# Kernel optimization log

Measured on AMD Instinct MI355X. Metric: run time of the kernel, lower is better.

Reference implementation:

```python
import jax, jax.numpy as jnp
import numpy as np

EPS = 1e-8          # torch nn.CosineSimilarity default eps
DIST_THR = 31.5     # 0.7 * 45 (module default)


def setup_inputs() -> dict:
    key = jax.random.key(0)
    k1, k2, k3, k4, k5 = jax.random.split(key, 5)
    B, C, H, W = 8, 256, 48, 48
    y = jax.random.normal(k1, (B, C, H, W), dtype=jnp.float32)
    yp = jax.random.normal(k2, (B, C, H, W), dtype=jnp.float32)
    z = jax.random.normal(k3, (B, C, H, W), dtype=jnp.float32)
    zp = jax.random.normal(k4, (B, C, H, W), dtype=jnp.float32)
    # distances in [0, 63): threshold 31.5 selects ~half of the pairs
    distances = jax.random.uniform(k5, (H, W, H, W), dtype=jnp.float32) * 63.0
    return {"y": y, "yp": yp, "z": z, "zp": zp, "distances": distances}


def _pairwise_cosine(a, b):
    # a, b: [B, C, N]; returns [B, N, N] cosine similarity over channel dim,
    # equivalent to CosineSimilarity(dim=1)(a[..., None], b[..., None, :])
    # but without materializing the [B, C, N, N] broadcast intermediate.
    dots = jnp.einsum('bcn,bcm->bnm', a, b)                       # [B,N,N]
    na = jnp.maximum(jnp.linalg.norm(a, axis=1), EPS)             # [B,N]
    nb = jnp.maximum(jnp.linalg.norm(b, axis=1), EPS)             # [B,N]
    return dots / (na[:, :, None] * nb[:, None, :])


def reference(y, yp, z, zp, distances):
    B, C = y.shape[0], y.shape[1]
    yf = y.reshape(B, C, -1)    # [B,C,N]
    ypf = yp.reshape(B, C, -1)
    zf = z.reshape(B, C, -1)
    zpf = zp.reshape(B, C, -1)

    cos_y_zp = _pairwise_cosine(yf, zpf)   # [B,N,N]
    cos_yp_z = _pairwise_cosine(zf, ypf)   # [B,N,N]

    H1, W1, H2, W2 = distances.shape
    mask = (distances.reshape(H1 * W1, H2 * W2) < DIST_THR)       # [N,N]

    # masked_select with mask broadcast over batch, then mean:
    # mean over B * count(mask) selected elements of -(cos1 + cos2)
    s = jnp.sum(jnp.where(mask[None, :, :], cos_y_zp + cos_yp_z, 0.0))
    cnt = jnp.sum(mask).astype(s.dtype) * B
    return -s / cnt
```

## Files before the change

kernel.cpp:

```cpp
#include <hip/hip_runtime.h>
#include <stdint.h>

#define GLOBAL_AS __attribute__((address_space(1)))
#define LDS_AS __attribute__((address_space(3)))

typedef _Float16 half_t;
typedef _Float16 f16x8 __attribute__((ext_vector_type(8)));
typedef float f32x4 __attribute__((ext_vector_type(4)));

static constexpr int BATCH = 8;
static constexpr int CH = 256;
static constexpr int N = 2304;
static constexpr int KTOT = 4096;
static constexpr int MW = 72;
static constexpr int MWORDS = 165888;
static constexpr int LROW = 258;
static constexpr float EPS = 1e-8f;
static constexpr float THR = 31.5f;


__global__ __launch_bounds__(256) void prep_kernel(
    const float* __restrict__ y, const float* __restrict__ yp,
    const float* __restrict__ z, const float* __restrict__ zp,
    const float* __restrict__ dist,
    half_t* __restrict__ At, half_t* __restrict__ Bt,
    uint32_t* __restrict__ maskw, unsigned int* __restrict__ c_part) {
  const int t = threadIdx.x;
  const int bz = blockIdx.z;

  if (bz >= 4) {
    const int blk = ((bz - 4) * 8 + blockIdx.y) * 36 + blockIdx.x;
    const int w = blk * 256 + t;
    int c = 0;
    if (w < MWORDS) {
      const float4* p = (const float4*)(dist + (size_t)w * 32);
      uint32_t bits = 0;
#pragma unroll
      for (int q = 0; q < 8; ++q) {
        float4 v = p[q];
        bits |= (v.x < THR ? 1u : 0u) << (q * 4);
        bits |= (v.y < THR ? 1u : 0u) << (q * 4 + 1);
        bits |= (v.z < THR ? 1u : 0u) << (q * 4 + 2);
        bits |= (v.w < THR ? 1u : 0u) << (q * 4 + 3);
      }
      maskw[w] = bits;
      c = __popc(bits);
    }
#pragma unroll
    for (int off = 32; off; off >>= 1) c += __shfl_down(c, off, 64);
    __shared__ int mred[4];
    if ((t & 63) == 0) mred[t >> 6] = c;
    __syncthreads();
    if (t == 0)
      c_part[blk] = (unsigned int)(mred[0] + mred[1] + mred[2] + mred[3]);
    return;
  }

  const int b = blockIdx.y;
  const int n0 = blockIdx.x * 64;
  const float* src; half_t* dst; int kh;
  switch (bz) {
    case 0:  src = y;  dst = At; kh = 0;    break;
    case 1:  src = z;  dst = At; kh = 2048; break;
    case 2:  src = zp; dst = Bt; kh = 0;    break;
    default: src = yp; dst = Bt; kh = 2048; break;
  }
  const int kbase = kh + b * 256;
  const int col4 = (t & 15) * 4;
  const int cb = t >> 4;

  const float* base = src + (size_t)(b * CH + cb * 16) * N + n0 + col4;
  float4 v[16];
#pragma unroll
  for (int i = 0; i < 16; ++i) v[i] = *(const float4*)(base + (size_t)i * N);

  float ss[4] = {0.f, 0.f, 0.f, 0.f};
#pragma unroll
  for (int i = 0; i < 16; ++i) {
    ss[0] = fmaf(v[i].x, v[i].x, ss[0]);
    ss[1] = fmaf(v[i].y, v[i].y, ss[1]);
    ss[2] = fmaf(v[i].z, v[i].z, ss[2]);
    ss[3] = fmaf(v[i].w, v[i].w, ss[3]);
  }
  __shared__ float partial[16][65];
  __shared__ float sc[64];
  __shared__ half_t tile[64 * LROW];
#pragma unroll
  for (int j = 0; j < 4; ++j) partial[cb][col4 + j] = ss[j];
  __syncthreads();
  if (t < 64) {
    float s = 0.f;
#pragma unroll
    for (int k = 0; k < 16; ++k) s += partial[k][t];
    sc[t] = 1.0f / fmaxf(sqrtf(s), EPS);
  }
  __syncthreads();

#pragma unroll
  for (int j = 0; j < 4; ++j) {
    const float scj = sc[col4 + j];
    union { half_t h[16]; f16x8 v2[2]; } u;
#pragma unroll
    for (int i = 0; i < 16; ++i)
      u.h[i] = (half_t)(((const float*)&v[i])[j] * scj);
    f16x8* q = (f16x8*)(tile + (col4 + j) * LROW + cb * 16);
    q[0] = u.v2[0];
    q[1] = u.v2[1];
  }
  __syncthreads();

  {
    const int r = t >> 4, c = t & 15;
#pragma unroll
    for (int p = 0; p < 4; ++p) {
      const int row = p * 16 + r;
      half_t* gout = dst + (size_t)(n0 + row) * KTOT + kbase;
      const half_t* lrow = tile + row * LROW;
#pragma unroll
      for (int inst = 0; inst < 2; ++inst) {
        const int off = c * 8 + inst * 128;
        *(f16x8*)(gout + off) = *(const f16x8*)(lrow + off);
      }
    }
  }
}

__global__ __launch_bounds__(256, 2) void gemm_kernel(
    const half_t* __restrict__ At, const half_t* __restrict__ Bt,
    const uint32_t* __restrict__ maskw, float* __restrict__ s_part) {
  __shared__ half_t As[128 * 64];
  __shared__ half_t Bs[256 * 64];
  __shared__ float red[4];

  const int t = threadIdx.x;
  const int lane = t & 63;
  const int w = t >> 6;

  const int bi = blockIdx.x;
  const int zt = bi & 7;
  const int v  = bi >> 3;
  const int nt = v / 9;
  const int mt = v % 9;
  const int m0 = mt * 256;
  const int n0 = nt * 128;
  const int k0 = zt * 512;

  const int srow = lane >> 3;
  const int schunk = ((lane & 7) ^ ((lane >> 3) & 7)) * 8;
  const half_t* gA = At + (size_t)(n0 + w * 32 + srow) * KTOT + k0 + schunk;
  const half_t* gB = Bt + (size_t)(m0 + w * 64 + srow) * KTOT + k0 + schunk;
  half_t* lA = As + (w * 32) * 64;
  half_t* lB = Bs + (w * 64) * 64;

  const int wm = (w & 1) * 64;
  const int wn = (w >> 1) * 128;
  const int fra = wm + (lane & 15);
  const int frb = wn + (lane & 15);
  const int fk0 = (((lane >> 4)    ) ^ (lane & 7)) * 8;
  const int fk1 = ((4 + (lane >> 4)) ^ (lane & 7)) * 8;

  f32x4 acc[4][8] = {};

  for (int kt = 0; kt < 8; ++kt) {
    const half_t* ga = gA + kt * 64;
    const half_t* gb = gB + kt * 64;
#pragma unroll
    for (int i = 0; i < 4; ++i)
      __builtin_amdgcn_global_load_lds((const GLOBAL_AS void*)(ga + (size_t)(i * 8) * KTOT),
                                       (LDS_AS void*)(lA + i * 8 * 64), 16, 0, 0);
#pragma unroll
    for (int i = 0; i < 8; ++i)
      __builtin_amdgcn_global_load_lds((const GLOBAL_AS void*)(gb + (size_t)(i * 8) * KTOT),
                                       (LDS_AS void*)(lB + i * 8 * 64), 16, 0, 0);
    __syncthreads();
#pragma unroll
    for (int s = 0; s < 2; ++s) {
      const int fk = s ? fk1 : fk0;
      f16x8 af[4], bf[8];
#pragma unroll
      for (int i = 0; i < 4; ++i) af[i] = *(const f16x8*)(As + (fra + i * 16) * 64 + fk);
#pragma unroll
      for (int j = 0; j < 8; ++j) bf[j] = *(const f16x8*)(Bs + (frb + j * 16) * 64 + fk);
#pragma unroll
      for (int i = 0; i < 4; ++i)
#pragma unroll
        for (int j = 0; j < 8; ++j)
          acc[i][j] = __builtin_amdgcn_mfma_f32_16x16x32_f16(af[i], bf[j], acc[i][j], 0, 0, 0);
    }
    __syncthreads();
  }

  float local = 0.f;
  const int mbase = (m0 + wn) >> 5;
  const int mbit = lane & 15;
#pragma unroll
  for (int i = 0; i < 4; ++i) {
    const int ng = n0 + wm + i * 16 + (lane >> 4) * 4;
#pragma unroll
    for (int r = 0; r < 4; ++r) {
      const uint4 wv = *(const uint4*)(maskw + (size_t)(ng + r) * MW + mbase);
      const uint32_t ww[4] = {wv.x, wv.y, wv.z, wv.w};
#pragma unroll
      for (int jp = 0; jp < 4; ++jp) {
        if ((ww[jp] >> mbit) & 1u)        local += acc[i][2 * jp][r];
        if ((ww[jp] >> (mbit + 16)) & 1u) local += acc[i][2 * jp + 1][r];
      }
    }
  }
#pragma unroll
  for (int off = 32; off; off >>= 1) local += __shfl_down(local, off, 64);
  if (lane == 0) red[w] = local;
  __syncthreads();
  if (t == 0) s_part[bi] = red[0] + red[1] + red[2] + red[3];
}

__global__ void finalize_kernel(const float* __restrict__ s_part,
                                const unsigned int* __restrict__ c_part,
                                float* __restrict__ out) {
  const int t = threadIdx.x;
  float local = 0.f;
  for (int i = t; i < 1296; i += 256) local += s_part[i];
  unsigned int clocal = 0;
  for (int i = t; i < 864; i += 256) clocal += c_part[i];
#pragma unroll
  for (int off = 32; off; off >>= 1) {
    local += __shfl_down(local, off, 64);
    clocal += __shfl_down(clocal, off, 64);
  }
  __shared__ float red[4];
  __shared__ unsigned int credu[4];
  if ((t & 63) == 0) { red[t >> 6] = local; credu[t >> 6] = clocal; }
  __syncthreads();
  if (t == 0) {
    const float s = red[0] + red[1] + red[2] + red[3];
    const float cnt = (float)(credu[0] + credu[1] + credu[2] + credu[3]);
    out[0] = -s / (cnt * (float)BATCH);
  }
}

extern "C" void kernel_launch(void* const* d_in, const int* in_sizes, int n_in,
                              void* d_out, int out_size, void* d_ws, size_t ws_size,
                              hipStream_t stream) {
  const float* y    = (const float*)d_in[0];
  const float* yp   = (const float*)d_in[1];
  const float* z    = (const float*)d_in[2];
  const float* zp   = (const float*)d_in[3];
  const float* dist = (const float*)d_in[4];
  float* out = (float*)d_out;

  char* ws = (char*)d_ws;
  float* s_part = (float*)ws;
  unsigned int* c_part = (unsigned int*)(ws + 8192);
  half_t* At = (half_t*)(ws + 16384);
  half_t* Bt = (half_t*)(ws + 16384 + 18874368);
  uint32_t* maskw = (uint32_t*)(ws + 16384 + 2 * 18874368);

  prep_kernel<<<dim3(36, 8, 7), 256, 0, stream>>>(y, yp, z, zp, dist, At, Bt, maskw, c_part);
  gemm_kernel<<<dim3(1296), 256, 0, stream>>>(At, Bt, maskw, s_part);
  finalize_kernel<<<1, 256, 0, stream>>>(s_part, c_part, out);
}
```

Baseline: 177.4 us.

## Restructure masked GEMM as 256x256 tiles with 4-stage LDS pipeline and 3-way split-K

The GEMM kernel moves from 1296 blocks of 128x256 tiles with 8-way split-K and a synchronous load-compute loop to 243 blocks of 512 threads computing 256x256 tiles with 3-way split-K. K steps of 32 go through a 4-buffer LDS ring filled by async global_load_lds, with explicit vmcnt waits, MFMA priority raising, and XCD-aware block remapping. The aim is to hide global load latency, raise data reuse per tile, and cut partial-sum overhead. In exchange it uses more LDS and registers per block, and 243 blocks may not fill all CUs evenly.

```diff
diff --git a/kernel.cpp b/kernel.cpp
--- a/kernel.cpp
+++ b/kernel.cpp
@@ -17,6 +17,7 @@
 static constexpr int LROW = 258;
 static constexpr float EPS = 1e-8f;
 static constexpr float THR = 31.5f;
+static constexpr int NBLK = 243;
 
 
 __global__ __launch_bounds__(256) void prep_kernel(
@@ -125,93 +126,111 @@
   }
 }
 
-__global__ __launch_bounds__(256, 2) void gemm_kernel(
+__global__ __launch_bounds__(512, 2) void gemm_kernel(
     const half_t* __restrict__ At, const half_t* __restrict__ Bt,
     const uint32_t* __restrict__ maskw, float* __restrict__ s_part) {
-  __shared__ half_t As[128 * 64];
-  __shared__ half_t Bs[256 * 64];
-  __shared__ float red[4];
+  __shared__ __align__(16) half_t As[4 * 8192];
+  __shared__ __align__(16) half_t Bs[4 * 8192];
+  __shared__ float red[8];
 
   const int t = threadIdx.x;
   const int lane = t & 63;
-  const int w = t >> 6;
-
-  const int bi = blockIdx.x;
-  const int zt = bi & 7;
-  const int v  = bi >> 3;
-  const int nt = v / 9;
-  const int mt = v % 9;
-  const int m0 = mt * 256;
-  const int n0 = nt * 128;
-  const int k0 = zt * 512;
-
-  const int srow = lane >> 3;
-  const int schunk = ((lane & 7) ^ ((lane >> 3) & 7)) * 8;
-  const half_t* gA = At + (size_t)(n0 + w * 32 + srow) * KTOT + k0 + schunk;
-  const half_t* gB = Bt + (size_t)(m0 + w * 64 + srow) * KTOT + k0 + schunk;
-  half_t* lA = As + (w * 32) * 64;
-  half_t* lB = Bs + (w * 64) * 64;
-
-  const int wm = (w & 1) * 64;
-  const int wn = (w >> 1) * 128;
-  const int fra = wm + (lane & 15);
-  const int frb = wn + (lane & 15);
-  const int fk0 = (((lane >> 4)    ) ^ (lane & 7)) * 8;
-  const int fk1 = ((4 + (lane >> 4)) ^ (lane & 7)) * 8;
-
-  f32x4 acc[4][8] = {};
-
-  for (int kt = 0; kt < 8; ++kt) {
-    const half_t* ga = gA + kt * 64;
-    const half_t* gb = gB + kt * 64;
-#pragma unroll
-    for (int i = 0; i < 4; ++i)
-      __builtin_amdgcn_global_load_lds((const GLOBAL_AS void*)(ga + (size_t)(i * 8) * KTOT),
-                                       (LDS_AS void*)(lA + i * 8 * 64), 16, 0, 0);
-#pragma unroll
-    for (int i = 0; i < 8; ++i)
-      __builtin_amdgcn_global_load_lds((const GLOBAL_AS void*)(gb + (size_t)(i * 8) * KTOT),
-                                       (LDS_AS void*)(lB + i * 8 * 64), 16, 0, 0);
-    __syncthreads();
-#pragma unroll
-    for (int s = 0; s < 2; ++s) {
-      const int fk = s ? fk1 : fk0;
-      f16x8 af[4], bf[8];
-#pragma unroll
-      for (int i = 0; i < 4; ++i) af[i] = *(const f16x8*)(As + (fra + i * 16) * 64 + fk);
-#pragma unroll
-      for (int j = 0; j < 8; ++j) bf[j] = *(const f16x8*)(Bs + (frb + j * 16) * 64 + fk);
-#pragma unroll
-      for (int i = 0; i < 4; ++i)
-#pragma unroll
-        for (int j = 0; j < 8; ++j)
-          acc[i][j] = __builtin_amdgcn_mfma_f32_16x16x32_f16(af[i], bf[j], acc[i][j], 0, 0, 0);
-    }
-    __syncthreads();
-  }
+  const int w8 = t >> 6;
+
+  const int orig = blockIdx.x;
+  const int xcd = orig & 7;
+  const int wid = (xcd < 3 ? xcd * 31 : 93 + (xcd - 3) * 30) + (orig >> 3);
+  const int zt = wid / 81;
+  const int t81 = wid % 81;
+  const int n0 = (t81 / 9) * 256;
+  const int m0 = (t81 % 9) * 256;
+  const int k0 = zt * 1376;
+  const int NT = 43 - (zt == 2);
+
+  const int srow = t >> 2;
+  const int schunk = ((t & 3) ^ ((srow >> 1) & 3)) * 8;
+  const half_t* gA = At + (size_t)(n0 + srow) * KTOT + k0 + schunk;
+  const half_t* gB = Bt + (size_t)(m0 + srow) * KTOT + k0 + schunk;
+
+  auto stage = [&](int j) {
+    const int buf = j & 3;
+    const half_t* ga = gA + j * 32;
+    const half_t* gb = gB + j * 32;
+    half_t* la = As + buf * 8192 + w8 * 512;
+    half_t* lb = Bs + buf * 8192 + w8 * 512;
+    __builtin_amdgcn_global_load_lds((const GLOBAL_AS void*)ga, (LDS_AS void*)la, 16, 0, 0);
+    __builtin_amdgcn_global_load_lds((const GLOBAL_AS void*)(ga + (size_t)128 * KTOT),
+                                     (LDS_AS void*)(la + 128 * 32), 16, 0, 0);
+    __builtin_amdgcn_global_load_lds((const GLOBAL_AS void*)gb, (LDS_AS void*)lb, 16, 0, 0);
+    __builtin_amdgcn_global_load_lds((const GLOBAL_AS void*)(gb + (size_t)128 * KTOT),
+                                     (LDS_AS void*)(lb + 128 * 32), 16, 0, 0);
+  };
+
+  const int fr = lane & 15;
+  const int clog = lane >> 4;
+  const int wA = w8 >> 2;
+  const int wB = w8 & 3;
+  const int ksw = (clog ^ ((fr >> 1) & 3)) * 8;
+  const int aoff = (wA * 128 + fr) * 32 + ksw;
+  const int boff = (wB * 64 + fr) * 32 + ksw;
+
+  f32x4 acc[8][4] = {};
+
+#define GEMM_TILE(KT, VMSTR, DO_STAGE)                                         \
+  {                                                                            \
+    asm volatile("s_waitcnt " VMSTR ::: "memory");                             \
+    __builtin_amdgcn_s_barrier();                                              \
+    asm volatile("" ::: "memory");                                             \
+    if (DO_STAGE) stage((KT) + 3);                                             \
+    const half_t* Ab = As + ((KT) & 3) * 8192;                                 \
+    const half_t* Bb = Bs + ((KT) & 3) * 8192;                                 \
+    f16x8 af[8], bf[4];                                                        \
+    _Pragma("unroll") for (int j = 0; j < 4; ++j)                              \
+        bf[j] = *(const f16x8*)(Bb + boff + j * 512);                          \
+    _Pragma("unroll") for (int i = 0; i < 8; ++i)                              \
+        af[i] = *(const f16x8*)(Ab + aoff + i * 512);                          \
+    __builtin_amdgcn_s_setprio(1);                                             \
+    _Pragma("unroll") for (int i = 0; i < 8; ++i)                              \
+      _Pragma("unroll") for (int j = 0; j < 4; ++j)                            \
+        acc[i][j] =                                                            \
+            __builtin_amdgcn_mfma_f32_16x16x32_f16(af[i], bf[j], acc[i][j], 0, 0, 0); \
+    __builtin_amdgcn_s_setprio(0);                                             \
+  }
+
+  stage(0); stage(1); stage(2);
+
+  int kt = 0;
+  for (; kt < NT - 3; ++kt) GEMM_TILE(kt, "vmcnt(8)", true);
+  GEMM_TILE(kt, "vmcnt(8)", false); ++kt;
+  GEMM_TILE(kt, "vmcnt(4)", false); ++kt;
+  GEMM_TILE(kt, "vmcnt(0)", false);
+#undef GEMM_TILE
 
   float local = 0.f;
-  const int mbase = (m0 + wn) >> 5;
-  const int mbit = lane & 15;
-#pragma unroll
-  for (int i = 0; i < 4; ++i) {
-    const int ng = n0 + wm + i * 16 + (lane >> 4) * 4;
+  const int mw0 = (m0 + wB * 64) >> 5;
+#pragma unroll
+  for (int i = 0; i < 8; ++i) {
+    const int ng = n0 + wA * 128 + i * 16 + clog * 4;
 #pragma unroll
     for (int r = 0; r < 4; ++r) {
-      const uint4 wv = *(const uint4*)(maskw + (size_t)(ng + r) * MW + mbase);
-      const uint32_t ww[4] = {wv.x, wv.y, wv.z, wv.w};
-#pragma unroll
-      for (int jp = 0; jp < 4; ++jp) {
-        if ((ww[jp] >> mbit) & 1u)        local += acc[i][2 * jp][r];
-        if ((ww[jp] >> (mbit + 16)) & 1u) local += acc[i][2 * jp + 1][r];
+      const uint2 wv = *(const uint2*)(maskw + (size_t)(ng + r) * MW + mw0);
+#pragma unroll
+      for (int j = 0; j < 4; ++j) {
+        const uint32_t ww = (j & 2) ? wv.y : wv.x;
+        if ((ww >> (fr + ((j & 1) << 4))) & 1u) local += acc[i][j][r];
       }
     }
   }
 #pragma unroll
   for (int off = 32; off; off >>= 1) local += __shfl_down(local, off, 64);
-  if (lane == 0) red[w] = local;
-  __syncthreads();
-  if (t == 0) s_part[bi] = red[0] + red[1] + red[2] + red[3];
+  if (lane == 0) red[w8] = local;
+  __syncthreads();
+  if (t == 0) {
+    float s = 0.f;
+#pragma unroll
+    for (int k = 0; k < 8; ++k) s += red[k];
+    s_part[orig] = s;
+  }
 }
 
 __global__ void finalize_kernel(const float* __restrict__ s_part,
@@ -219,7 +238,7 @@
                                 float* __restrict__ out) {
   const int t = threadIdx.x;
   float local = 0.f;
-  for (int i = t; i < 1296; i += 256) local += s_part[i];
+  for (int i = t; i < NBLK; i += 256) local += s_part[i];
   unsigned int clocal = 0;
   for (int i = t; i < 864; i += 256) clocal += c_part[i];
 #pragma unroll
@@ -256,6 +275,6 @@
   uint32_t* maskw = (uint32_t*)(ws + 16384 + 2 * 18874368);
 
   prep_kernel<<<dim3(36, 8, 7), 256, 0, stream>>>(y, yp, z, zp, dist, At, Bt, maskw, c_part);
-  gemm_kernel<<<dim3(1296), 256, 0, stream>>>(At, Bt, maskw, s_part);
+  gemm_kernel<<<dim3(NBLK), 512, 0, stream>>>(At, Bt, maskw, s_part);
   finalize_kernel<<<1, 256, 0, stream>>>(s_part, c_part, out);
 }
```

Result: slower. 182.6 us (+2.9%).
